# Kernel tuning notes

Hardware: AMD Instinct MI355X
Metric: run time of the kernel (lower is better)

## Reference

```python
import jax, jax.numpy as jnp
import numpy as np

B, N, IN_DIM, OUT_DIM = 16, 2048, 512, 512

def _xavier(key, shape):
    bound = float(np.sqrt(6.0 / (shape[0] + shape[1])))
    return jax.random.uniform(key, shape, jnp.float32, -bound, bound)

def setup_inputs() -> dict:
    key = jax.random.key(0)
    kx, kk, kq, kv = jax.random.split(key, 4)
    return {
        "x": jax.random.normal(kx, (B, N, IN_DIM), jnp.float32),
        "W_key": _xavier(kk, (IN_DIM, OUT_DIM)),
        "W_query": _xavier(kq, (IN_DIM, OUT_DIM)),
        "W_value": _xavier(kv, (IN_DIM, OUT_DIM)),
    }

def reference(x, W_key, W_query, W_value):
    # projections: [B, N, out_dim]
    k = jnp.matmul(x, W_key)
    q = jnp.matmul(x, W_query)
    v = jnp.matmul(x, W_value)
    scale = jnp.sqrt(jnp.asarray(IN_DIM, jnp.float32))
    scores = jnp.einsum("bnd,bmd->bnm", q, k) / scale  # [B, N, N]
    weights = jax.nn.softmax(scores, axis=2)
    attn = jnp.einsum("bnm,bmd->bnd", weights, v)  # [B, N, out_dim]
    return jnp.mean(attn, axis=1)  # [B, out_dim]
```

## Files before the change

kernel.cpp:

```cpp
#include <hip/hip_runtime.h>
#include <hip/hip_bf16.h>
#include <hip/hip_fp16.h>
#include <stdint.h>

#define NB 16
#define NN 2048
#define ND 512
#define LDQKV 1536
#define SSCALE 0.044194173824159216f

typedef unsigned short u16;
typedef unsigned int u32;
typedef float f32x4 __attribute__((ext_vector_type(4)));
typedef __bf16 bf16x8 __attribute__((ext_vector_type(8)));
typedef unsigned short u16x8 __attribute__((ext_vector_type(8)));

__device__ __forceinline__ float bf2f(u16 h) {
  union { u32 u; float f; } v; v.u = ((u32)h) << 16; return v.f;
}
__device__ __forceinline__ u16 f2bf(float f) {
  union { float f; u32 u; } v; v.f = f;
  u32 r = v.u + 0x7fffu + ((v.u >> 16) & 1u);
  return (u16)(r >> 16);
}
__device__ __forceinline__ u16 f2h(float f) {
  __half h = __float2half(f);
  union { __half h; u16 u; } v; v.h = h; return v.u;
}

__device__ __forceinline__ void async16(const void* g, void* l) {
  __builtin_amdgcn_global_load_lds(
      (const __attribute__((address_space(1))) u32*)g,
      (__attribute__((address_space(3))) u32*)l,
      16, 0, 0);
}

template <int MODE, bool AF32>
__global__ __launch_bounds__(256, 2) void gemm_bt(
    const void* __restrict__ Av, const u16* __restrict__ B, u16* __restrict__ C,
    float* __restrict__ Lrow, int lda, int ldb, int ldc, int K,
    long long sA, long long sB, long long sC, float cscale) {
  const int tid  = threadIdx.x;
  const int w    = tid >> 6;
  const int lane = tid & 63;
  const int wm   = w >> 1, wn = w & 1;
  const int lrow = lane & 15, quad = lane >> 4;
  const long long z = blockIdx.z;

  const float* Abf = (const float*)Av + z * sA + (size_t)blockIdx.y * 128 * lda;
  const u16*   Abh = (const u16*)Av   + z * sA + (size_t)blockIdx.y * 128 * lda;
  const u16*   Bb  = B + z * sB + (size_t)blockIdx.x * 128 * ldb;

  __shared__ __align__(16) u16 lds_a[128 * 32];
  __shared__ __align__(16) u16 lds_b[128 * 32];

  f32x4 acc[4][4];
#pragma unroll
  for (int i = 0; i < 4; i++)
#pragma unroll
    for (int j = 0; j < 4; j++) acc[i][j] = (f32x4){0.f, 0.f, 0.f, 0.f};

  for (int k0 = 0; k0 < K; k0 += 32) {
    if (k0) __syncthreads();
    if (AF32) {
      u16x8 va[2];
#pragma unroll
      for (int t = 0; t < 2; t++) {
        int ch  = t * 256 + tid;
        int row = ch >> 2;
        int cc  = (ch & 3) * 8;
        const float4* p = (const float4*)(Abf + (size_t)row * lda + k0 + cc);
        float4 f0 = p[0], f1 = p[1];
        u16x8 r;
        r[0] = f2bf(f0.x); r[1] = f2bf(f0.y); r[2] = f2bf(f0.z); r[3] = f2bf(f0.w);
        r[4] = f2bf(f1.x); r[5] = f2bf(f1.y); r[6] = f2bf(f1.z); r[7] = f2bf(f1.w);
        va[t] = r;
        async16(Bb + (size_t)row * ldb + k0 + cc, &lds_b[ch * 8]);
      }
#pragma unroll
      for (int t = 0; t < 2; t++) *(u16x8*)&lds_a[(t * 256 + tid) * 8] = va[t];
    } else {
#pragma unroll
      for (int t = 0; t < 2; t++) {
        int ch  = t * 256 + tid;
        int row = ch >> 2;
        int cc  = (ch & 3) * 8;
        async16(Abh + (size_t)row * lda + k0 + cc, &lds_a[ch * 8]);
        async16(Bb  + (size_t)row * ldb + k0 + cc, &lds_b[ch * 8]);
      }
    }
    __syncthreads();

    bf16x8 af[4], bfr[4];
#pragma unroll
    for (int i = 0; i < 4; i++) {
      af[i]  = *(const bf16x8*)&lds_a[(wm * 64 + i * 16 + lrow) * 32 + quad * 8];
      bfr[i] = *(const bf16x8*)&lds_b[(wn * 64 + i * 16 + lrow) * 32 + quad * 8];
    }
#pragma unroll
    for (int i = 0; i < 4; i++)
#pragma unroll
      for (int j = 0; j < 4; j++)
        acc[i][j] =
            __builtin_amdgcn_mfma_f32_16x16x32_bf16(af[i], bfr[j], acc[i][j], 0, 0, 0);
  }

  u16* Cb = C + z * sC + (size_t)blockIdx.y * 128 * ldc + (size_t)blockIdx.x * 128;
  if (MODE == 0) {
#pragma unroll
    for (int i = 0; i < 4; i++)
#pragma unroll
      for (int j = 0; j < 4; j++)
#pragma unroll
        for (int r = 0; r < 4; r++) {
          int row = wm * 64 + i * 16 + quad * 4 + r;
          int col = wn * 64 + j * 16 + lrow;
          Cb[(size_t)row * ldc + col] = f2bf(acc[i][j][r] * cscale);
        }
  } else {
    float* Lb = Lrow + z * NN + (size_t)blockIdx.y * 128;
#pragma unroll
    for (int i = 0; i < 4; i++)
#pragma unroll
      for (int r = 0; r < 4; r++) {
        int row = wm * 64 + i * 16 + quad * 4 + r;
        float rs = 0.f;
#pragma unroll
        for (int j = 0; j < 4; j++) {
          int col = wn * 64 + j * 16 + lrow;
          float e = __expf(fminf(acc[i][j][r] * cscale, 10.f));
          Cb[(size_t)row * ldc + col] = f2h(e);
          rs += e;
        }
        rs += __shfl_xor(rs, 1); rs += __shfl_xor(rs, 2);
        rs += __shfl_xor(rs, 4); rs += __shfl_xor(rs, 8);
        if (lrow == 0) atomicAdd(&Lb[row], rs);
      }
  }
}

__global__ void cast_x(const float* __restrict__ x, u16* __restrict__ xb) {
  size_t i = ((size_t)blockIdx.x * 256 + threadIdx.x) * 8;
  float4 f0 = *(const float4*)(x + i);
  float4 f1 = *(const float4*)(x + i + 4);
  u16x8 r;
  r[0] = f2bf(f0.x); r[1] = f2bf(f0.y); r[2] = f2bf(f0.z); r[3] = f2bf(f0.w);
  r[4] = f2bf(f1.x); r[5] = f2bf(f1.y); r[6] = f2bf(f1.z); r[7] = f2bf(f1.w);
  *(u16x8*)(xb + i) = r;
}

__global__ void transpose_w(const float* __restrict__ Wq, const float* __restrict__ Wk,
                            const float* __restrict__ Wv, u16* __restrict__ Wt) {
  __shared__ u16 t[32][33];
  const float* W = blockIdx.z == 0 ? Wq : (blockIdx.z == 1 ? Wk : Wv);
  u16* dst = Wt + (size_t)blockIdx.z * 512 * 512;
  int n0 = blockIdx.x * 32, k0 = blockIdx.y * 32;
  int tx = threadIdx.x, ty = threadIdx.y;
  for (int r = ty; r < 32; r += 8)
    t[r][tx] = f2bf(W[(size_t)(k0 + r) * 512 + n0 + tx]);
  __syncthreads();
  for (int r = ty; r < 32; r += 8)
    dst[(size_t)(n0 + r) * 512 + k0 + tx] = t[tx][r];
}

__global__ void recip_k(const float* __restrict__ L, float* __restrict__ InvL) {
  int i = blockIdx.x * 256 + threadIdx.x;
  InvL[i] = 1.0f / L[i];
}

__global__ void col_sum(const __half* __restrict__ E, const float* __restrict__ InvL,
                        float* __restrict__ c) {
  int m2 = blockIdx.x * 256 + threadIdx.x;
  int n0 = blockIdx.y * 128;
  int z  = blockIdx.z;
  const __half2* Ep = (const __half2*)(E + ((size_t)z * NN + n0) * NN) + m2;
  const float* lp = InvL + (size_t)z * NN + n0;
  float a0 = 0.f, a1 = 0.f;
#pragma unroll 4
  for (int n = 0; n < 128; n++) {
    __half2 h = Ep[(size_t)n * (NN / 2)];
    float il = lp[n];
    a0 += __low2float(h) * il;
    a1 += __high2float(h) * il;
  }
  atomicAdd(&c[(size_t)z * NN + m2 * 2], a0);
  atomicAdd(&c[(size_t)z * NN + m2 * 2 + 1], a1);
}

__global__ void out_accum(const u16* __restrict__ qkv, const float* __restrict__ c,
                          float* __restrict__ cout) {
  int b = blockIdx.x, mc = blockIdx.y, t = threadIdx.x;
  const u16* vp = qkv + ((size_t)b * NN + mc * 128) * LDQKV + 1024;
  const float* cp = c + b * NN + mc * 128;
  float a0 = 0.f, a1 = 0.f;
#pragma unroll 4
  for (int m = 0; m < 128; m++) {
    float cm = cp[m];
    a0 += cm * bf2f(vp[(size_t)m * LDQKV + t]);
    a1 += cm * bf2f(vp[(size_t)m * LDQKV + 256 + t]);
  }
  atomicAdd(&cout[b * ND + t], a0);
  atomicAdd(&cout[b * ND + 256 + t], a1);
}

__global__ void finalize_k(const float* __restrict__ cout, float* __restrict__ out) {
  int i = blockIdx.x * 256 + threadIdx.x;
  out[i] = cout[i] * (1.f / (float)NN);
}

extern "C" void kernel_launch(void* const* d_in, const int* in_sizes, int n_in,
                              void* d_out, int out_size, void* d_ws, size_t ws_size,
                              hipStream_t stream) {
  const float* x  = (const float*)d_in[0];
  const float* Wk = (const float*)d_in[1];
  const float* Wq = (const float*)d_in[2];
  const float* Wv = (const float*)d_in[3];
  float* out = (float*)d_out;

  char* ws = (char*)d_ws;
  size_t off = 0;
  float* L    = (float*)(ws + off); off += (size_t)NB * NN * 4;
  float* c    = (float*)(ws + off); off += (size_t)NB * NN * 4;
  float* cout = (float*)(ws + off); off += (size_t)NB * ND * 4;
  float* InvL = (float*)(ws + off); off += (size_t)NB * NN * 4;
  u16* Wt     = (u16*)(ws + off);   off += (size_t)LDQKV * ND * 2;
  const size_t small_total = off;

  const size_t QKV16 = (size_t)NB * NN * LDQKV * 2;
  const size_t QKV1  = (size_t)NN * LDQKV * 2;
  const size_t SB1   = (size_t)NN * NN * 2;
  const size_t XBSZ  = (size_t)NB * NN * ND * 2;
  size_t avail = ws_size > small_total ? ws_size - small_total : 0;
  int nbq; size_t qkvsz;
  if (avail >= QKV16 + (size_t)128 * NN * 2) { nbq = 16; qkvsz = QKV16; }
  else                                       { nbq = 1;  qkvsz = QKV1;  }
  u16* qkv  = (u16*)(ws + small_total);
  char* big = ws + small_total + qkvsz;
  size_t srem = avail > qkvsz ? avail - qkvsz : 0;
  bool use_xb = (nbq == 16) && (srem >= XBSZ);
  u16* xb = (u16*)big;
  __half* E = (__half*)big;
  int chb = 0, sr = 128;
  if (nbq == 16) {
    if      (srem >= 4 * SB1) chb = 4;
    else if (srem >= 2 * SB1) chb = 2;
    else if (srem >= 1 * SB1) chb = 1;
  }
  if (chb == 0) {
    if      (srem >= SB1)                   sr = 2048;
    else if (srem >= (size_t)1024 * NN * 2) sr = 1024;
    else if (srem >= (size_t)512  * NN * 2) sr = 512;
    else if (srem >= (size_t)256  * NN * 2) sr = 256;
  }

  hipMemsetAsync(L, 0, (size_t)(2 * NB * NN + NB * ND) * sizeof(float), stream);

  transpose_w<<<dim3(16, 16, 3), dim3(32, 8), 0, stream>>>(Wq, Wk, Wv, Wt);

  const long long sQKV = (long long)NN * LDQKV;
  const long long sS   = (long long)NN * NN;

  if (nbq == 16) {
    if (use_xb) {
      cast_x<<<8192, 256, 0, stream>>>(x, xb);
      gemm_bt<0, false><<<dim3(12, 256, 1), 256, 0, stream>>>(
          xb, Wt, qkv, nullptr, ND, ND, LDQKV, ND, 0, 0, 0, 1.0f);
    } else {
      gemm_bt<0, true><<<dim3(12, 256, 1), 256, 0, stream>>>(
          x, Wt, qkv, nullptr, ND, ND, LDQKV, ND, 0, 0, 0, 1.0f);
    }
    if (chb >= 1) {
      const int CH = chb;
      for (int cc = 0; cc < NB / CH; ++cc) {
        const u16* qb = qkv + (size_t)cc * CH * sQKV;
        size_t o = (size_t)cc * CH * NN;
        gemm_bt<1, false><<<dim3(16, 16, CH), 256, 0, stream>>>(
            qb, qb + 512, (u16*)E, L + o, LDQKV, LDQKV, NN, ND,
            sQKV, sQKV, sS, SSCALE);
        recip_k<<<CH * NN / 256, 256, 0, stream>>>(L + o, InvL + o);
        col_sum<<<dim3(4, 16, CH), 256, 0, stream>>>(E, InvL + o, c + o);
      }
    } else {
      for (int b = 0; b < NB; ++b) {
        const u16* qb = qkv + (size_t)b * sQKV;
        for (int ch = 0; ch < NN / sr; ++ch) {
          size_t o = (size_t)b * NN + (size_t)ch * sr;
          gemm_bt<1, false><<<dim3(16, sr / 128, 1), 256, 0, stream>>>(
              qb + (size_t)ch * sr * LDQKV, qb + 512, (u16*)E, L + o - 0,
              LDQKV, LDQKV, NN, ND, 0, 0, 0, SSCALE);
          recip_k<<<sr / 256, 256, 0, stream>>>(L + o, InvL + o);
          col_sum<<<dim3(4, sr / 128, 1), 256, 0, stream>>>(E, InvL + o, c + b * NN);
        }
      }
    }
    out_accum<<<dim3(16, 16), 256, 0, stream>>>(qkv, c, cout);
  } else {
    for (int b = 0; b < NB; ++b) {
      gemm_bt<0, true><<<dim3(12, 16, 1), 256, 0, stream>>>(
          x + (size_t)b * NN * ND, Wt, qkv, nullptr, ND, ND, LDQKV, ND,
          0, 0, 0, 1.0f);
      for (int ch = 0; ch < NN / sr; ++ch) {
        size_t o = (size_t)b * NN + (size_t)ch * sr;
        gemm_bt<1, false><<<dim3(16, sr / 128, 1), 256, 0, stream>>>(
            qkv + (size_t)ch * sr * LDQKV, qkv + 512, (u16*)E, L + o,
            LDQKV, LDQKV, NN, ND, 0, 0, 0, SSCALE);
        recip_k<<<sr / 256, 256, 0, stream>>>(L + o, InvL + o);
        col_sum<<<dim3(4, sr / 128, 1), 256, 0, stream>>>(E, InvL + o, c + b * NN);
      }
      out_accum<<<dim3(1, 16), 256, 0, stream>>>(qkv, c + b * NN, cout + b * ND);
    }
  }

  finalize_k<<<32, 256, 0, stream>>>(cout, out);
  (void)in_sizes; (void)n_in; (void)out_size;
}
```

Baseline: 386.9 us.

## Fold Q/K projections into one Wq·Wkᵀ matrix and apply Wv after reduction

Scores are rewritten as x·M·xᵀ with M = scale·Wq·Wkᵀ, computed once as a small GEMM. Only y = x·M is projected, replacing the three 512-wide Q/K/V projections. The value projection is applied after the column-weighted sum over rows, as a tiny per-batch matvec. The reciprocal and finalize kernels are folded into neighbouring kernels, and larger batch chunks are allowed when workspace permits. This removes most of the projection GEMM work and several launches, but bf16 rounding of M may change accuracy.

```diff
diff --git a/kernel.cpp b/kernel.cpp
--- a/kernel.cpp
+++ b/kernel.cpp
@@ -6,7 +6,6 @@
 #define NB 16
 #define NN 2048
 #define ND 512
-#define LDQKV 1536
 #define SSCALE 0.044194173824159216f
 
 typedef unsigned short u16;
@@ -139,7 +138,7 @@
   }
 }
 
-__global__ void cast_x(const float* __restrict__ x, u16* __restrict__ xb) {
+__global__ void cast_f32_bf16(const float* __restrict__ x, u16* __restrict__ xb) {
   size_t i = ((size_t)blockIdx.x * 256 + threadIdx.x) * 8;
   float4 f0 = *(const float4*)(x + i);
   float4 f1 = *(const float4*)(x + i + 4);
@@ -149,37 +148,18 @@
   *(u16x8*)(xb + i) = r;
 }
 
-__global__ void transpose_w(const float* __restrict__ Wq, const float* __restrict__ Wk,
-                            const float* __restrict__ Wv, u16* __restrict__ Wt) {
-  __shared__ u16 t[32][33];
-  const float* W = blockIdx.z == 0 ? Wq : (blockIdx.z == 1 ? Wk : Wv);
-  u16* dst = Wt + (size_t)blockIdx.z * 512 * 512;
-  int n0 = blockIdx.x * 32, k0 = blockIdx.y * 32;
-  int tx = threadIdx.x, ty = threadIdx.y;
-  for (int r = ty; r < 32; r += 8)
-    t[r][tx] = f2bf(W[(size_t)(k0 + r) * 512 + n0 + tx]);
-  __syncthreads();
-  for (int r = ty; r < 32; r += 8)
-    dst[(size_t)(n0 + r) * 512 + k0 + tx] = t[tx][r];
-}
-
-__global__ void recip_k(const float* __restrict__ L, float* __restrict__ InvL) {
-  int i = blockIdx.x * 256 + threadIdx.x;
-  InvL[i] = 1.0f / L[i];
-}
-
-__global__ void col_sum(const __half* __restrict__ E, const float* __restrict__ InvL,
+__global__ void col_sum(const __half* __restrict__ E, const float* __restrict__ L,
                         float* __restrict__ c) {
   int m2 = blockIdx.x * 256 + threadIdx.x;
   int n0 = blockIdx.y * 128;
   int z  = blockIdx.z;
   const __half2* Ep = (const __half2*)(E + ((size_t)z * NN + n0) * NN) + m2;
-  const float* lp = InvL + (size_t)z * NN + n0;
+  const float* lp = L + (size_t)z * NN + n0;
   float a0 = 0.f, a1 = 0.f;
 #pragma unroll 4
   for (int n = 0; n < 128; n++) {
     __half2 h = Ep[(size_t)n * (NN / 2)];
-    float il = lp[n];
+    float il = 1.0f / lp[n];
     a0 += __low2float(h) * il;
     a1 += __high2float(h) * il;
   }
@@ -187,25 +167,30 @@
   atomicAdd(&c[(size_t)z * NN + m2 * 2 + 1], a1);
 }
 
-__global__ void out_accum(const u16* __restrict__ qkv, const float* __restrict__ c,
-                          float* __restrict__ cout) {
-  int b = blockIdx.x, mc = blockIdx.y, t = threadIdx.x;
-  const u16* vp = qkv + ((size_t)b * NN + mc * 128) * LDQKV + 1024;
+__global__ void tx_accum(const u16* __restrict__ xb, const float* __restrict__ c,
+                         float* __restrict__ t) {
+  int b = blockIdx.x, mc = blockIdx.y, d = threadIdx.x;
+  const u16* vp = xb + ((size_t)b * NN + mc * 128) * ND;
   const float* cp = c + b * NN + mc * 128;
   float a0 = 0.f, a1 = 0.f;
 #pragma unroll 4
   for (int m = 0; m < 128; m++) {
     float cm = cp[m];
-    a0 += cm * bf2f(vp[(size_t)m * LDQKV + t]);
-    a1 += cm * bf2f(vp[(size_t)m * LDQKV + 256 + t]);
-  }
-  atomicAdd(&cout[b * ND + t], a0);
-  atomicAdd(&cout[b * ND + 256 + t], a1);
-}
-
-__global__ void finalize_k(const float* __restrict__ cout, float* __restrict__ out) {
-  int i = blockIdx.x * 256 + threadIdx.x;
-  out[i] = cout[i] * (1.f / (float)NN);
+    a0 += cm * bf2f(vp[(size_t)m * ND + d]);
+    a1 += cm * bf2f(vp[(size_t)m * ND + 256 + d]);
+  }
+  atomicAdd(&t[b * ND + d], a0);
+  atomicAdd(&t[b * ND + 256 + d], a1);
+}
+
+__global__ void final_wv(const float* __restrict__ t, const float* __restrict__ Wv,
+                         float* __restrict__ out) {
+  int b = blockIdx.x, d = blockIdx.y * 256 + threadIdx.x;
+  const float* tb = t + b * ND;
+  float a = 0.f;
+#pragma unroll 4
+  for (int l = 0; l < ND; l++) a += tb[l] * Wv[(size_t)l * ND + d];
+  out[b * ND + d] = a * (1.f / (float)NN);
 }
 
 extern "C" void kernel_launch(void* const* d_in, const int* in_sizes, int n_in,
@@ -219,98 +204,67 @@
 
   char* ws = (char*)d_ws;
   size_t off = 0;
-  float* L    = (float*)(ws + off); off += (size_t)NB * NN * 4;
-  float* c    = (float*)(ws + off); off += (size_t)NB * NN * 4;
-  float* cout = (float*)(ws + off); off += (size_t)NB * ND * 4;
-  float* InvL = (float*)(ws + off); off += (size_t)NB * NN * 4;
-  u16* Wt     = (u16*)(ws + off);   off += (size_t)LDQKV * ND * 2;
+  float* L   = (float*)(ws + off); off += (size_t)NB * NN * 4;
+  float* c   = (float*)(ws + off); off += (size_t)NB * NN * 4;
+  float* t   = (float*)(ws + off); off += (size_t)NB * ND * 4;
+  u16* Wqb   = (u16*)(ws + off);   off += (size_t)ND * ND * 2;
+  u16* Mt    = (u16*)(ws + off);   off += (size_t)ND * ND * 2;
   const size_t small_total = off;
 
-  const size_t QKV16 = (size_t)NB * NN * LDQKV * 2;
-  const size_t QKV1  = (size_t)NN * LDQKV * 2;
-  const size_t SB1   = (size_t)NN * NN * 2;
-  const size_t XBSZ  = (size_t)NB * NN * ND * 2;
-  size_t avail = ws_size > small_total ? ws_size - small_total : 0;
-  int nbq; size_t qkvsz;
-  if (avail >= QKV16 + (size_t)128 * NN * 2) { nbq = 16; qkvsz = QKV16; }
-  else                                       { nbq = 1;  qkvsz = QKV1;  }
-  u16* qkv  = (u16*)(ws + small_total);
-  char* big = ws + small_total + qkvsz;
-  size_t srem = avail > qkvsz ? avail - qkvsz : 0;
-  bool use_xb = (nbq == 16) && (srem >= XBSZ);
-  u16* xb = (u16*)big;
-  __half* E = (__half*)big;
+  const size_t XBSZ = (size_t)NB * NN * ND * 2;
+  const size_t SB1  = (size_t)NN * NN * 2;
+  u16* xb   = (u16*)(ws + small_total);
+  u16* y    = (u16*)(ws + small_total + XBSZ);
+  __half* E = (__half*)(ws + small_total + 2 * XBSZ);
+  size_t srem = ws_size > small_total + 2 * XBSZ
+              ? ws_size - small_total - 2 * XBSZ : 0;
   int chb = 0, sr = 128;
-  if (nbq == 16) {
-    if      (srem >= 4 * SB1) chb = 4;
-    else if (srem >= 2 * SB1) chb = 2;
-    else if (srem >= 1 * SB1) chb = 1;
-  }
-  if (chb == 0) {
-    if      (srem >= SB1)                   sr = 2048;
-    else if (srem >= (size_t)1024 * NN * 2) sr = 1024;
+  if      (srem >= 16 * SB1) chb = 16;
+  else if (srem >=  8 * SB1) chb = 8;
+  else if (srem >=  4 * SB1) chb = 4;
+  else if (srem >=  2 * SB1) chb = 2;
+  else if (srem >=  1 * SB1) chb = 1;
+  else {
+    if      (srem >= (size_t)1024 * NN * 2) sr = 1024;
     else if (srem >= (size_t)512  * NN * 2) sr = 512;
     else if (srem >= (size_t)256  * NN * 2) sr = 256;
   }
 
   hipMemsetAsync(L, 0, (size_t)(2 * NB * NN + NB * ND) * sizeof(float), stream);
 
-  transpose_w<<<dim3(16, 16, 3), dim3(32, 8), 0, stream>>>(Wq, Wk, Wv, Wt);
-
-  const long long sQKV = (long long)NN * LDQKV;
-  const long long sS   = (long long)NN * NN;
-
-  if (nbq == 16) {
-    if (use_xb) {
-      cast_x<<<8192, 256, 0, stream>>>(x, xb);
-      gemm_bt<0, false><<<dim3(12, 256, 1), 256, 0, stream>>>(
-          xb, Wt, qkv, nullptr, ND, ND, LDQKV, ND, 0, 0, 0, 1.0f);
-    } else {
-      gemm_bt<0, true><<<dim3(12, 256, 1), 256, 0, stream>>>(
-          x, Wt, qkv, nullptr, ND, ND, LDQKV, ND, 0, 0, 0, 1.0f);
-    }
-    if (chb >= 1) {
-      const int CH = chb;
-      for (int cc = 0; cc < NB / CH; ++cc) {
-        const u16* qb = qkv + (size_t)cc * CH * sQKV;
-        size_t o = (size_t)cc * CH * NN;
-        gemm_bt<1, false><<<dim3(16, 16, CH), 256, 0, stream>>>(
-            qb, qb + 512, (u16*)E, L + o, LDQKV, LDQKV, NN, ND,
-            sQKV, sQKV, sS, SSCALE);
-        recip_k<<<CH * NN / 256, 256, 0, stream>>>(L + o, InvL + o);
-        col_sum<<<dim3(4, 16, CH), 256, 0, stream>>>(E, InvL + o, c + o);
-      }
-    } else {
-      for (int b = 0; b < NB; ++b) {
-        const u16* qb = qkv + (size_t)b * sQKV;
-        for (int ch = 0; ch < NN / sr; ++ch) {
-          size_t o = (size_t)b * NN + (size_t)ch * sr;
-          gemm_bt<1, false><<<dim3(16, sr / 128, 1), 256, 0, stream>>>(
-              qb + (size_t)ch * sr * LDQKV, qb + 512, (u16*)E, L + o - 0,
-              LDQKV, LDQKV, NN, ND, 0, 0, 0, SSCALE);
-          recip_k<<<sr / 256, 256, 0, stream>>>(L + o, InvL + o);
-          col_sum<<<dim3(4, sr / 128, 1), 256, 0, stream>>>(E, InvL + o, c + b * NN);
-        }
-      }
-    }
-    out_accum<<<dim3(16, 16), 256, 0, stream>>>(qkv, c, cout);
+  cast_f32_bf16<<<8192, 256, 0, stream>>>(x, xb);
+  cast_f32_bf16<<<128, 256, 0, stream>>>(Wq, Wqb);
+
+  gemm_bt<0, true><<<dim3(4, 4, 1), 256, 0, stream>>>(
+      Wk, Wqb, Mt, nullptr, ND, ND, ND, ND, 0, 0, 0, SSCALE);
+
+  gemm_bt<0, false><<<dim3(4, 256, 1), 256, 0, stream>>>(
+      xb, Mt, y, nullptr, ND, ND, ND, ND, 0, 0, 0, 1.0f);
+
+  const long long sR = (long long)NN * ND;
+  const long long sS = (long long)NN * NN;
+
+  if (chb >= 1) {
+    for (int cc = 0; cc < NB / chb; ++cc) {
+      size_t o = (size_t)cc * chb * NN;
+      gemm_bt<1, false><<<dim3(16, 16, chb), 256, 0, stream>>>(
+          y + o * ND, xb + o * ND, (u16*)E, L + o, ND, ND, NN, ND,
+          sR, sR, sS, 1.0f);
+      col_sum<<<dim3(4, 16, chb), 256, 0, stream>>>(E, L + o, c + o);
+    }
   } else {
     for (int b = 0; b < NB; ++b) {
-      gemm_bt<0, true><<<dim3(12, 16, 1), 256, 0, stream>>>(
-          x + (size_t)b * NN * ND, Wt, qkv, nullptr, ND, ND, LDQKV, ND,
-          0, 0, 0, 1.0f);
       for (int ch = 0; ch < NN / sr; ++ch) {
         size_t o = (size_t)b * NN + (size_t)ch * sr;
         gemm_bt<1, false><<<dim3(16, sr / 128, 1), 256, 0, stream>>>(
-            qkv + (size_t)ch * sr * LDQKV, qkv + 512, (u16*)E, L + o,
-            LDQKV, LDQKV, NN, ND, 0, 0, 0, SSCALE);
-        recip_k<<<sr / 256, 256, 0, stream>>>(L + o, InvL + o);
-        col_sum<<<dim3(4, sr / 128, 1), 256, 0, stream>>>(E, InvL + o, c + b * NN);
-      }
-      out_accum<<<dim3(1, 16), 256, 0, stream>>>(qkv, c + b * NN, cout + b * ND);
-    }
-  }
-
-  finalize_k<<<32, 256, 0, stream>>>(cout, out);
+            y + o * ND, xb + (size_t)b * NN * ND, (u16*)E, L + o,
+            ND, ND, NN, ND, 0, 0, 0, 1.0f);
+        col_sum<<<dim3(4, sr / 128, 1), 256, 0, stream>>>(E, L + o, c + b * NN);
+      }
+    }
+  }
+
+  tx_accum<<<dim3(NB, 16), 256, 0, stream>>>(xb, c, t);
+  final_wv<<<dim3(NB, 2), 256, 0, stream>>>(t, Wv, out);
   (void)in_sizes; (void)n_in; (void)out_size;
 }
```

New measurement: 360.6 us. 6.8% less time.
